# Optimization experiments

Hardware: AMD Instinct MI355X
Metric: run time of the kernel (lower is better)

## Reference

```python
import jax, jax.numpy as jnp
import numpy as np

B, CAPS, FEAT = 16384, 32, 256


def setup_inputs() -> dict:
    key = jax.random.key(0)
    k1, k2 = jax.random.split(key)
    inputs = jax.random.normal(k1, (B, CAPS, FEAT), dtype=jnp.float32)
    bias = jax.random.normal(k2, (CAPS, FEAT), dtype=jnp.float32) * 0.02
    return {"inputs": inputs, "bias": bias}


def reference(inputs, bias):
    # inputs: [B, caps, feat]; bias: [caps, feat]
    num_features = inputs.shape[-1]
    # self-similarity: scores[b, i] = sum_{k, j} inputs[b,i,j] * inputs[b,k,j]
    scores = jnp.einsum('bij,bkj->bi', inputs, inputs) / jnp.sqrt(
        jnp.asarray(num_features, dtype=inputs.dtype))
    # softmax over capsule dim (dim=-2 of [..., i, 1] == i), then broadcast-add bias
    attn = jax.nn.softmax(scores, axis=-1)[..., None] + bias  # [B, caps, feat]
    # weighted sum over capsules; activation is Identity
    return (inputs * attn).sum(axis=1)  # [B, feat]
```

## Files before the change

### kernel.cpp

```cpp
#include <hip/hip_runtime.h>
#include <math.h>


constexpr int CAPS = 32;
constexpr int FEAT = 256;

__global__ __launch_bounds__(256, 4)
void router_kernel(const float* __restrict__ inp,
                   const float* __restrict__ bias,
                   float* __restrict__ out) {
    const int b    = blockIdx.x;
    const int t    = threadIdx.x;
    const int f    = t & 63;
    const int w    = t >> 6;

    const float4* inp4  = reinterpret_cast<const float4*>(inp + (size_t)b * CAPS * FEAT);
    const float4* bias4 = reinterpret_cast<const float4*>(bias);

    __shared__ float4 red_lds[4][64];
    __shared__ float  scores_lds[CAPS];
    __shared__ float  sm_lds[CAPS];

    float4 x[8];
    #pragma unroll
    for (int il = 0; il < 8; ++il) {
        const int i = w * 8 + il;
        x[il] = inp4[i * (FEAT / 4) + f];
    }

    float4 pc = x[0];
    #pragma unroll
    for (int il = 1; il < 8; ++il) {
        pc.x += x[il].x; pc.y += x[il].y; pc.z += x[il].z; pc.w += x[il].w;
    }
    red_lds[w][f] = pc;
    __syncthreads();
    float4 cs = red_lds[0][f];
    {
        const float4 a = red_lds[1][f];
        const float4 c = red_lds[2][f];
        const float4 d = red_lds[3][f];
        cs.x += a.x + c.x + d.x;
        cs.y += a.y + c.y + d.y;
        cs.z += a.z + c.z + d.z;
        cs.w += a.w + c.w + d.w;
    }

    float p[8];
    #pragma unroll
    for (int il = 0; il < 8; ++il) {
        p[il] = x[il].x * cs.x + x[il].y * cs.y + x[il].z * cs.z + x[il].w * cs.w;
    }
    #pragma unroll
    for (int step = 1; step < 64; step <<= 1) {
        #pragma unroll
        for (int il = 0; il < 8; ++il)
            p[il] += __shfl_xor(p[il], step, 64);
    }
    if (f == 0) {
        #pragma unroll
        for (int il = 0; il < 8; ++il)
            scores_lds[w * 8 + il] = p[il];
    }
    __syncthreads();

    if (t < CAPS) {
        const float s = scores_lds[t] * 0.0625f;
        float m = s;
        #pragma unroll
        for (int step = 1; step < 32; step <<= 1)
            m = fmaxf(m, __shfl_xor(m, step, 64));
        const float e = __expf(s - m);
        float tot = e;
        #pragma unroll
        for (int step = 1; step < 32; step <<= 1)
            tot += __shfl_xor(tot, step, 64);
        sm_lds[t] = e / tot;
    }
    __syncthreads();

    float4 acc = make_float4(0.f, 0.f, 0.f, 0.f);
    #pragma unroll
    for (int il = 0; il < 8; ++il) {
        const int i = w * 8 + il;
        const float4 bv = bias4[i * (FEAT / 4) + f];
        const float  s  = sm_lds[i];
        acc.x += x[il].x * (s + bv.x);
        acc.y += x[il].y * (s + bv.y);
        acc.z += x[il].z * (s + bv.z);
        acc.w += x[il].w * (s + bv.w);
    }

    red_lds[w][f] = acc;
    __syncthreads();
    if (w == 0) {
        const float4 a0 = red_lds[0][f];
        const float4 a1 = red_lds[1][f];
        const float4 a2 = red_lds[2][f];
        const float4 a3 = red_lds[3][f];
        float4 o;
        o.x = a0.x + a1.x + a2.x + a3.x;
        o.y = a0.y + a1.y + a2.y + a3.y;
        o.z = a0.z + a1.z + a2.z + a3.z;
        o.w = a0.w + a1.w + a2.w + a3.w;
        reinterpret_cast<float4*>(out + (size_t)b * FEAT)[f] = o;
    }
}

extern "C" void kernel_launch(void* const* d_in, const int* in_sizes, int n_in,
                              void* d_out, int out_size, void* d_ws, size_t ws_size,
                              hipStream_t stream) {
    const float* inp  = reinterpret_cast<const float*>(d_in[0]);
    const float* bias = reinterpret_cast<const float*>(d_in[1]);
    float* out        = reinterpret_cast<float*>(d_out);

    const int batch = in_sizes[0] / (CAPS * FEAT);
    router_kernel<<<batch, 256, 0, stream>>>(inp, bias, out);
}
```

Before: 674.1 us.

## Persistent grid with register double-buffered prefetch and shuffle-based reductions

Measured after the change: 687.8 us. 1.02x slower.

```diff
diff --git a/kernel.cpp b/kernel.cpp
--- a/kernel.cpp
+++ b/kernel.cpp
@@ -4,106 +4,129 @@
 
 constexpr int CAPS = 32;
 constexpr int FEAT = 256;
+constexpr int F4   = FEAT / 4;
+constexpr int NBLK = 2048;
 
 __global__ __launch_bounds__(256, 4)
 void router_kernel(const float* __restrict__ inp,
                    const float* __restrict__ bias,
-                   float* __restrict__ out) {
-    const int b    = blockIdx.x;
+                   float* __restrict__ out, int batch) {
     const int t    = threadIdx.x;
-    const int f    = t & 63;
     const int w    = t >> 6;
+    const int lane = t & 63;
+    const int ci   = lane >> 4;
+    const int fi   = lane & 15;
+    const int g    = w * 16 + fi;
+    const int c    = lane & 31;
 
-    const float4* inp4  = reinterpret_cast<const float4*>(inp + (size_t)b * CAPS * FEAT);
+    __shared__ float pscore[2][4][CAPS];
+
+    const float4* inp4  = reinterpret_cast<const float4*>(inp);
     const float4* bias4 = reinterpret_cast<const float4*>(bias);
 
-    __shared__ float4 red_lds[4][64];
-    __shared__ float  scores_lds[CAPS];
-    __shared__ float  sm_lds[CAPS];
+    int rowoff[8];
+    #pragma unroll
+    for (int il = 0; il < 8; ++il) rowoff[il] = (8 * ci + il) * F4 + g;
 
-    float4 x[8];
-    #pragma unroll
-    for (int il = 0; il < 8; ++il) {
-        const int i = w * 8 + il;
-        x[il] = inp4[i * (FEAT / 4) + f];
+    const int G = gridDim.x;
+
+    auto process = [&](float4 (&x)[8], int b, int buf) {
+        float4 cs = x[0];
+        #pragma unroll
+        for (int il = 1; il < 8; ++il) {
+            cs.x += x[il].x; cs.y += x[il].y; cs.z += x[il].z; cs.w += x[il].w;
+        }
+        #pragma unroll
+        for (int m = 16; m <= 32; m <<= 1) {
+            cs.x += __shfl_xor(cs.x, m, 64);
+            cs.y += __shfl_xor(cs.y, m, 64);
+            cs.z += __shfl_xor(cs.z, m, 64);
+            cs.w += __shfl_xor(cs.w, m, 64);
+        }
+
+        float p[8];
+        #pragma unroll
+        for (int il = 0; il < 8; ++il)
+            p[il] = x[il].x * cs.x + x[il].y * cs.y + x[il].z * cs.z + x[il].w * cs.w;
+        #pragma unroll
+        for (int m = 1; m <= 8; m <<= 1) {
+            #pragma unroll
+            for (int il = 0; il < 8; ++il)
+                p[il] += __shfl_xor(p[il], m, 64);
+        }
+        if (fi == 0) {
+            float4* dst = reinterpret_cast<float4*>(&pscore[buf][w][ci * 8]);
+            dst[0] = make_float4(p[0], p[1], p[2], p[3]);
+            dst[1] = make_float4(p[4], p[5], p[6], p[7]);
+        }
+        asm volatile("s_waitcnt lgkmcnt(0)" ::: "memory");
+        __builtin_amdgcn_s_barrier();
+        asm volatile("" ::: "memory");
+
+        float s = (pscore[buf][0][c] + pscore[buf][1][c] +
+                   pscore[buf][2][c] + pscore[buf][3][c]) * 0.0625f;
+        float mx = s;
+        #pragma unroll
+        for (int m = 1; m <= 16; m <<= 1)
+            mx = fmaxf(mx, __shfl_xor(mx, m, 64));
+        const float e = __expf(s - mx);
+        float tot = e;
+        #pragma unroll
+        for (int m = 1; m <= 16; m <<= 1)
+            tot += __shfl_xor(tot, m, 64);
+        const float wgt = e / tot;
+
+        float4 acc = make_float4(0.f, 0.f, 0.f, 0.f);
+        #pragma unroll
+        for (int il = 0; il < 8; ++il) {
+            const float  wv = __shfl(wgt, ci * 8 + il, 64);
+            const float4 bv = bias4[rowoff[il]];
+            acc.x += x[il].x * (wv + bv.x);
+            acc.y += x[il].y * (wv + bv.y);
+            acc.z += x[il].z * (wv + bv.z);
+            acc.w += x[il].w * (wv + bv.w);
+        }
+        #pragma unroll
+        for (int m = 16; m <= 32; m <<= 1) {
+            acc.x += __shfl_xor(acc.x, m, 64);
+            acc.y += __shfl_xor(acc.y, m, 64);
+            acc.z += __shfl_xor(acc.z, m, 64);
+            acc.w += __shfl_xor(acc.w, m, 64);
+        }
+        if (ci == 0)
+            reinterpret_cast<float4*>(out + (size_t)b * FEAT)[g] = acc;
+    };
+
+    int b = blockIdx.x;
+    if (b >= batch) return;
+
+    float4 xa[8], xb[8];
+    {
+        const float4* src = inp4 + (size_t)b * (CAPS * F4);
+        #pragma unroll
+        for (int il = 0; il < 8; ++il) xa[il] = src[rowoff[il]];
     }
 
-    float4 pc = x[0];
-    #pragma unroll
-    for (int il = 1; il < 8; ++il) {
-        pc.x += x[il].x; pc.y += x[il].y; pc.z += x[il].z; pc.w += x[il].w;
-    }
-    red_lds[w][f] = pc;
-    __syncthreads();
-    float4 cs = red_lds[0][f];
-    {
-        const float4 a = red_lds[1][f];
-        const float4 c = red_lds[2][f];
-        const float4 d = red_lds[3][f];
-        cs.x += a.x + c.x + d.x;
-        cs.y += a.y + c.y + d.y;
-        cs.z += a.z + c.z + d.z;
-        cs.w += a.w + c.w + d.w;
-    }
+    for (;;) {
+        int b1 = b + G;
+        if (b1 < batch) {
+            const float4* src = inp4 + (size_t)b1 * (CAPS * F4);
+            #pragma unroll
+            for (int il = 0; il < 8; ++il) xb[il] = src[rowoff[il]];
+        }
+        process(xa, b, 0);
+        if (b1 >= batch) return;
+        b = b1;
 
-    float p[8];
-    #pragma unroll
-    for (int il = 0; il < 8; ++il) {
-        p[il] = x[il].x * cs.x + x[il].y * cs.y + x[il].z * cs.z + x[il].w * cs.w;
-    }
-    #pragma unroll
-    for (int step = 1; step < 64; step <<= 1) {
-        #pragma unroll
-        for (int il = 0; il < 8; ++il)
-            p[il] += __shfl_xor(p[il], step, 64);
-    }
-    if (f == 0) {
-        #pragma unroll
-        for (int il = 0; il < 8; ++il)
-            scores_lds[w * 8 + il] = p[il];
-    }
-    __syncthreads();
-
-    if (t < CAPS) {
-        const float s = scores_lds[t] * 0.0625f;
-        float m = s;
-        #pragma unroll
-        for (int step = 1; step < 32; step <<= 1)
-            m = fmaxf(m, __shfl_xor(m, step, 64));
-        const float e = __expf(s - m);
-        float tot = e;
-        #pragma unroll
-        for (int step = 1; step < 32; step <<= 1)
-            tot += __shfl_xor(tot, step, 64);
-        sm_lds[t] = e / tot;
-    }
-    __syncthreads();
-
-    float4 acc = make_float4(0.f, 0.f, 0.f, 0.f);
-    #pragma unroll
-    for (int il = 0; il < 8; ++il) {
-        const int i = w * 8 + il;
-        const float4 bv = bias4[i * (FEAT / 4) + f];
-        const float  s  = sm_lds[i];
-        acc.x += x[il].x * (s + bv.x);
-        acc.y += x[il].y * (s + bv.y);
-        acc.z += x[il].z * (s + bv.z);
-        acc.w += x[il].w * (s + bv.w);
-    }
-
-    red_lds[w][f] = acc;
-    __syncthreads();
-    if (w == 0) {
-        const float4 a0 = red_lds[0][f];
-        const float4 a1 = red_lds[1][f];
-        const float4 a2 = red_lds[2][f];
-        const float4 a3 = red_lds[3][f];
-        float4 o;
-        o.x = a0.x + a1.x + a2.x + a3.x;
-        o.y = a0.y + a1.y + a2.y + a3.y;
-        o.z = a0.z + a1.z + a2.z + a3.z;
-        o.w = a0.w + a1.w + a2.w + a3.w;
-        reinterpret_cast<float4*>(out + (size_t)b * FEAT)[f] = o;
+        int b2 = b + G;
+        if (b2 < batch) {
+            const float4* src = inp4 + (size_t)b2 * (CAPS * F4);
+            #pragma unroll
+            for (int il = 0; il < 8; ++il) xa[il] = src[rowoff[il]];
+        }
+        process(xb, b, 1);
+        if (b2 >= batch) return;
+        b = b2;
     }
 }
 
@@ -115,5 +138,6 @@
     float* out        = reinterpret_cast<float*>(d_out);
 
     const int batch = in_sizes[0] / (CAPS * FEAT);
-    router_kernel<<<batch, 256, 0, stream>>>(inp, bias, out);
+    const int grid  = (batch < NBLK) ? batch : NBLK;
+    router_kernel<<<grid, 256, 0, stream>>>(inp, bias, out, batch);
 }
```
